# Optimization experiments

Hardware: AMD Instinct MI355X
Metric: run time of the kernel (lower is better)

## Reference

```python
import jax, jax.numpy as jnp
import numpy as np

MAXDISP = 192
D = MAXDISP // 3  # 64 disparity levels at 1/3 resolution


def setup_inputs() -> dict:
    key = jax.random.key(0)
    k1, k2 = jax.random.split(key)
    B, C, H, W = 2, 32, 80, 240
    x = jax.random.normal(k1, (B, C, H, W), dtype=jnp.float32)  # left features
    y = jax.random.normal(k2, (B, C, H, W), dtype=jnp.float32)  # right features
    return {"x": x, "y": y}


def reference(x, y):
    # Faithful vectorization of:
    #   cost = zeros(B, 2C, D, H, W)
    #   for i in range(D):
    #       cost[:, :C, i, :, i:] = x[:, :, :, i:]
    #       cost[:, C:, i, :, i:] = y[:, :, :, :W-i]
    B, C, H, W = x.shape
    d = jnp.arange(D)                      # [D]
    w = jnp.arange(W)                      # [W]
    mask = (w[None, :] >= d[:, None]).astype(x.dtype)   # [D, W]; zero for w < disparity
    m = mask[None, None, :, None, :]                    # [1,1,D,1,W]

    # left half: x broadcast over disparity, masked
    left = x[:, :, None, :, :] * m                      # [B,C,D,H,W]

    # right half: y shifted right by d along W, masked
    idx = jnp.clip(w[None, :] - d[:, None], 0)          # [D, W]
    right = jnp.take(y, idx, axis=3)                    # [B,C,H,D,W]
    right = jnp.moveaxis(right, 3, 2) * m               # [B,C,D,H,W]

    return jnp.concatenate([left, right], axis=1)       # [B,2C,D,H,W]
```

## Files before the change

kernel.cpp:

```cpp
#include <hip/hip_runtime.h>


#define W4    60u
#define CH4   307200u
#define D4    4800u

__global__ __launch_bounds__(256) void costvol_kernel(const float* __restrict__ x,
                                                      const float* __restrict__ y,
                                                      float* __restrict__ out) {
    __shared__ float xs[240];
    __shared__ float ysbuf[64 + 240];

    const unsigned t  = threadIdx.x;
    const unsigned blk = blockIdx.x;
    const unsigned h  = blk % 80u;
    const unsigned bc = blk / 80u;
    const unsigned c  = bc % 32u;
    const unsigned b  = bc / 32u;

    const float4* xrow = (const float4*)(x + (size_t)blk * 240u);
    const float4* yrow = (const float4*)(y + (size_t)blk * 240u);

    if (t < 16u)                 ((float4*)ysbuf)[t]       = make_float4(0.f, 0.f, 0.f, 0.f);
    else if (t < 76u)            ((float4*)ysbuf)[t]       = yrow[t - 16u];
    if (t >= 128u && t < 188u)   ((float4*)xs)[t - 128u]   = xrow[t - 128u];
    __syncthreads();

    const float* ys = ysbuf + 64;
    float4* out4 = (float4*)out;
    const unsigned baseL = (b * 64u + c)       * CH4 + h * W4;
    const unsigned baseR = (b * 64u + 32u + c) * CH4 + h * W4;

    #pragma unroll
    for (unsigned it = 0; it < 15u; ++it) {
        unsigned i  = it * 256u + t;
        unsigned d  = i / 60u;
        unsigned qw = i - d * 60u;
        float4 v = ((const float4*)xs)[qw];
        int w0 = 4 * (int)qw, dd = (int)d;
        if (w0 + 0 < dd) v.x = 0.f;
        if (w0 + 1 < dd) v.y = 0.f;
        if (w0 + 2 < dd) v.z = 0.f;
        if (w0 + 3 < dd) v.w = 0.f;
        out4[baseL + d * D4 + qw] = v;
    }

    #pragma unroll
    for (unsigned it = 0; it < 15u; ++it) {
        unsigned i  = it * 256u + t;
        unsigned d  = i / 60u;
        unsigned qw = i - d * 60u;
        int s = 4 * (int)qw - (int)d;
        float4 v;
        v.x = ys[s + 0];
        v.y = ys[s + 1];
        v.z = ys[s + 2];
        v.w = ys[s + 3];
        out4[baseR + d * D4 + qw] = v;
    }
}

extern "C" void kernel_launch(void* const* d_in, const int* in_sizes, int n_in,
                              void* d_out, int out_size, void* d_ws, size_t ws_size,
                              hipStream_t stream) {
    const float* x = (const float*)d_in[0];
    const float* y = (const float*)d_in[1];
    float* out     = (float*)d_out;

    dim3 grid(2u * 32u * 80u), block(256);
    hipLaunchKernelGGL(costvol_kernel, grid, block, 0, stream, x, y, out);
}
```

Baseline: 649.7 us.

## Use nontemporal stores and per-wave disparity mapping with vectorized LDS splicing

Stores to the cost volume now use nontemporal hints so the write-only output does not pollute the caches. Each wave handles a fixed residue of disparity modulo 4 and each lane a fixed float4 column. This removes the per-element division and lets the shifted right half be built from two aligned float4 LDS reads spliced at a compile-time offset, instead of four scalar LDS reads. In exchange, 4 of every 64 lanes sit idle, and there is more template code plus an extra zero pad in shared memory.

```diff
diff --git a/kernel.cpp b/kernel.cpp
--- a/kernel.cpp
+++ b/kernel.cpp
@@ -5,58 +5,93 @@
 #define CH4   307200u
 #define D4    4800u
 
+typedef float f32x4 __attribute__((ext_vector_type(4)));
+
+__device__ __forceinline__ void nt_store4(float4 v, float4* p) {
+    f32x4 t; t.x = v.x; t.y = v.y; t.z = v.z; t.w = v.w;
+    __builtin_nontemporal_store(t, reinterpret_cast<f32x4*>(p));
+}
+
+template <int R>
+__device__ __forceinline__ float4 splice(float4 a, float4 b) {
+    if constexpr (R == 0)      return a;
+    else if constexpr (R == 1) return make_float4(a.y, a.z, a.w, b.x);
+    else if constexpr (R == 2) return make_float4(a.z, a.w, b.x, b.y);
+    else                       return make_float4(a.w, b.x, b.y, b.z);
+}
+
+template <int R>
+__device__ __forceinline__ void right_half(const float4* __restrict__ yq,
+                                           float4* __restrict__ out4,
+                                           unsigned lane, unsigned wv,
+                                           unsigned baseR) {
+    unsigned qa  = (64u + 4u * lane - wv - (unsigned)R) >> 2;
+    unsigned off = baseR + wv * D4 + lane;
+    float4 q1 = yq[qa + 1u];
+    float4 q0 = yq[qa];
+    #pragma unroll
+    for (unsigned k = 0; k < 16u; ++k) {
+        nt_store4(splice<R>(q0, q1), &out4[off]);
+        off += 4u * D4;
+        q1 = q0;
+        if (k + 1u < 16u) q0 = yq[--qa];
+    }
+}
+
 __global__ __launch_bounds__(256) void costvol_kernel(const float* __restrict__ x,
                                                       const float* __restrict__ y,
                                                       float* __restrict__ out) {
-    __shared__ float xs[240];
-    __shared__ float ysbuf[64 + 240];
+    __shared__ __align__(16) float xs[240];
+    __shared__ __align__(16) float ysbuf[308];
 
-    const unsigned t  = threadIdx.x;
+    const unsigned t   = threadIdx.x;
     const unsigned blk = blockIdx.x;
-    const unsigned h  = blk % 80u;
-    const unsigned bc = blk / 80u;
-    const unsigned c  = bc % 32u;
-    const unsigned b  = bc / 32u;
+    const unsigned h   = blk % 80u;
+    const unsigned bc  = blk / 80u;
+    const unsigned c   = bc % 32u;
+    const unsigned b   = bc / 32u;
 
     const float4* xrow = (const float4*)(x + (size_t)blk * 240u);
     const float4* yrow = (const float4*)(y + (size_t)blk * 240u);
+    float4* xsq = (float4*)xs;
+    float4* ysq = (float4*)ysbuf;
 
-    if (t < 16u)                 ((float4*)ysbuf)[t]       = make_float4(0.f, 0.f, 0.f, 0.f);
-    else if (t < 76u)            ((float4*)ysbuf)[t]       = yrow[t - 16u];
-    if (t >= 128u && t < 188u)   ((float4*)xs)[t - 128u]   = xrow[t - 128u];
+    if (t < 16u)                 ysq[t]        = make_float4(0.f, 0.f, 0.f, 0.f);
+    else if (t < 76u)            ysq[t]        = yrow[t - 16u];
+    else if (t == 76u)           ysq[76]       = make_float4(0.f, 0.f, 0.f, 0.f);
+    if (t >= 128u && t < 188u)   xsq[t - 128u] = xrow[t - 128u];
     __syncthreads();
 
-    const float* ys = ysbuf + 64;
+    const unsigned lane = t & 63u;
+    const unsigned wv   = t >> 6;
+    if (lane >= 60u) return;
+
     float4* out4 = (float4*)out;
-    const unsigned baseL = (b * 64u + c)       * CH4 + h * W4;
-    const unsigned baseR = (b * 64u + 32u + c) * CH4 + h * W4;
+    const unsigned baseL = (b * 64u + c) * CH4 + h * W4;
+    const unsigned baseR = baseL + 32u * CH4;
 
-    #pragma unroll
-    for (unsigned it = 0; it < 15u; ++it) {
-        unsigned i  = it * 256u + t;
-        unsigned d  = i / 60u;
-        unsigned qw = i - d * 60u;
-        float4 v = ((const float4*)xs)[qw];
-        int w0 = 4 * (int)qw, dd = (int)d;
-        if (w0 + 0 < dd) v.x = 0.f;
-        if (w0 + 1 < dd) v.y = 0.f;
-        if (w0 + 2 < dd) v.z = 0.f;
-        if (w0 + 3 < dd) v.w = 0.f;
-        out4[baseL + d * D4 + qw] = v;
+    {
+        const float4 xv = xsq[lane];
+        const int w0 = 4 * (int)lane;
+        unsigned off = baseL + wv * D4 + lane;
+        #pragma unroll
+        for (unsigned k = 0; k < 16u; ++k) {
+            const int d = (int)(wv + 4u * k);
+            float4 v = xv;
+            if (w0 + 0 < d) v.x = 0.f;
+            if (w0 + 1 < d) v.y = 0.f;
+            if (w0 + 2 < d) v.z = 0.f;
+            if (w0 + 3 < d) v.w = 0.f;
+            nt_store4(v, &out4[off]);
+            off += 4u * D4;
+        }
     }
 
-    #pragma unroll
-    for (unsigned it = 0; it < 15u; ++it) {
-        unsigned i  = it * 256u + t;
-        unsigned d  = i / 60u;
-        unsigned qw = i - d * 60u;
-        int s = 4 * (int)qw - (int)d;
-        float4 v;
-        v.x = ys[s + 0];
-        v.y = ys[s + 1];
-        v.z = ys[s + 2];
-        v.w = ys[s + 3];
-        out4[baseR + d * D4 + qw] = v;
+    switch (wv) {
+        case 0:  right_half<0>(ysq, out4, lane, wv, baseR); break;
+        case 1:  right_half<3>(ysq, out4, lane, wv, baseR); break;
+        case 2:  right_half<2>(ysq, out4, lane, wv, baseR); break;
+        default: right_half<1>(ysq, out4, lane, wv, baseR); break;
     }
 }
 
```

New measurement: 622.5 us. 1.04x faster.

## Remap blocks to output planes with nontemporal stores and register splicing

Applied to the files above, without the earlier changes.

Each block now writes one contiguous (batch, channel, disparity) output plane instead of one input row across all disparities. Input rows are read directly from global memory, with no shared-memory staging, and shifted using a compile-time splice of two float4 loads. Block indices are swizzled so that blocks for the same input channel land on the same XCD. Output is written with nontemporal stores to avoid polluting the cache. The trade-off is repeated global reads of each input plane, 64 times per channel, which are expected to hit in L2.

```diff
diff --git a/kernel.cpp b/kernel.cpp
--- a/kernel.cpp
+++ b/kernel.cpp
@@ -1,62 +1,85 @@
 #include <hip/hip_runtime.h>
 
 
-#define W4    60u
-#define CH4   307200u
-#define D4    4800u
+#define NQP  4800u
+#define W4q  60u
+
+typedef float f32x4 __attribute__((ext_vector_type(4)));
+
+__device__ __forceinline__ void nt_store4(float4 v, float4* p) {
+    f32x4 t; t.x = v.x; t.y = v.y; t.z = v.z; t.w = v.w;
+    __builtin_nontemporal_store(t, reinterpret_cast<f32x4*>(p));
+}
+
+template <int SH>
+__device__ __forceinline__ float4 splice(float4 a, float4 b) {
+    if constexpr (SH == 1)      return make_float4(a.y, a.z, a.w, b.x);
+    else if constexpr (SH == 2) return make_float4(a.z, a.w, b.x, b.y);
+    else                        return make_float4(a.w, b.x, b.y, b.z);
+}
+
+template <int SH>
+__device__ __forceinline__ void right_path(const float4* __restrict__ src4,
+                                           float4* __restrict__ dst4,
+                                           unsigned t, unsigned k) {
+    const float4 zero = make_float4(0.f, 0.f, 0.f, 0.f);
+    for (unsigned i = t; i < NQP; i += 256u) {
+        const unsigned h  = i / W4q;
+        const unsigned qw = i - h * W4q;
+        const float4* row = src4 + h * W4q;
+        const int qb = (int)qw - (int)k;
+        float4 vb = (qb >= 0) ? row[qb] : zero;
+        float4 v;
+        if constexpr (SH == 0) {
+            v = vb;
+        } else {
+            const int qa = qb - 1;
+            float4 va = (qa >= 0) ? row[qa] : zero;
+            v = splice<SH>(va, vb);
+        }
+        nt_store4(v, &dst4[i]);
+    }
+}
 
 __global__ __launch_bounds__(256) void costvol_kernel(const float* __restrict__ x,
                                                       const float* __restrict__ y,
                                                       float* __restrict__ out) {
-    __shared__ float xs[240];
-    __shared__ float ysbuf[64 + 240];
+    const unsigned blk  = blockIdx.x;
+    const unsigned xcd  = blk & 7u;
+    const unsigned rest = blk >> 3;
+    const unsigned d    = rest & 63u;
+    const unsigned p    = (rest >> 6) * 8u + xcd;
+    const unsigned ch   = p & 63u;
+    const unsigned b    = p >> 6;
+    const unsigned c    = ch & 31u;
+    const bool right    = ch >= 32u;
 
-    const unsigned t  = threadIdx.x;
-    const unsigned blk = blockIdx.x;
-    const unsigned h  = blk % 80u;
-    const unsigned bc = blk / 80u;
-    const unsigned c  = bc % 32u;
-    const unsigned b  = bc / 32u;
+    const float4* src4 = (const float4*)(right ? y : x) + (size_t)(b * 32u + c) * NQP;
+    float4*       dst4 = (float4*)out + (size_t)(p * 64u + d) * NQP;
 
-    const float4* xrow = (const float4*)(x + (size_t)blk * 240u);
-    const float4* yrow = (const float4*)(y + (size_t)blk * 240u);
+    const unsigned t = threadIdx.x;
 
-    if (t < 16u)                 ((float4*)ysbuf)[t]       = make_float4(0.f, 0.f, 0.f, 0.f);
-    else if (t < 76u)            ((float4*)ysbuf)[t]       = yrow[t - 16u];
-    if (t >= 128u && t < 188u)   ((float4*)xs)[t - 128u]   = xrow[t - 128u];
-    __syncthreads();
-
-    const float* ys = ysbuf + 64;
-    float4* out4 = (float4*)out;
-    const unsigned baseL = (b * 64u + c)       * CH4 + h * W4;
-    const unsigned baseR = (b * 64u + 32u + c) * CH4 + h * W4;
-
-    #pragma unroll
-    for (unsigned it = 0; it < 15u; ++it) {
-        unsigned i  = it * 256u + t;
-        unsigned d  = i / 60u;
-        unsigned qw = i - d * 60u;
-        float4 v = ((const float4*)xs)[qw];
-        int w0 = 4 * (int)qw, dd = (int)d;
-        if (w0 + 0 < dd) v.x = 0.f;
-        if (w0 + 1 < dd) v.y = 0.f;
-        if (w0 + 2 < dd) v.z = 0.f;
-        if (w0 + 3 < dd) v.w = 0.f;
-        out4[baseL + d * D4 + qw] = v;
-    }
-
-    #pragma unroll
-    for (unsigned it = 0; it < 15u; ++it) {
-        unsigned i  = it * 256u + t;
-        unsigned d  = i / 60u;
-        unsigned qw = i - d * 60u;
-        int s = 4 * (int)qw - (int)d;
-        float4 v;
-        v.x = ys[s + 0];
-        v.y = ys[s + 1];
-        v.z = ys[s + 2];
-        v.w = ys[s + 3];
-        out4[baseR + d * D4 + qw] = v;
+    if (!right) {
+        const int dd = (int)d;
+        for (unsigned i = t; i < NQP; i += 256u) {
+            const unsigned h  = i / W4q;
+            const unsigned qw = i - h * W4q;
+            float4 v = src4[i];
+            const int w0 = 4 * (int)qw;
+            if (w0 + 0 < dd) v.x = 0.f;
+            if (w0 + 1 < dd) v.y = 0.f;
+            if (w0 + 2 < dd) v.z = 0.f;
+            if (w0 + 3 < dd) v.w = 0.f;
+            nt_store4(v, &dst4[i]);
+        }
+    } else {
+        const unsigned k = d >> 2;
+        switch (d & 3u) {
+            case 0:  right_path<0>(src4, dst4, t, k); break;
+            case 1:  right_path<3>(src4, dst4, t, k); break;
+            case 2:  right_path<2>(src4, dst4, t, k); break;
+            default: right_path<1>(src4, dst4, t, k); break;
+        }
     }
 }
 
@@ -67,6 +90,6 @@
     const float* y = (const float*)d_in[1];
     float* out     = (float*)d_out;
 
-    dim3 grid(2u * 32u * 80u), block(256);
+    dim3 grid(2u * 64u * 64u), block(256);
     hipLaunchKernelGGL(costvol_kernel, grid, block, 0, stream, x, y, out);
 }
```

Result: slower. 684.3 us (+5.3%).
